# Performance work log

Measured on AMD Instinct MI355X. Metric: run time of the kernel, lower is better.

The kernel has to match this reference:

```python
import jax, jax.numpy as jnp
import numpy as np

N_NODES = 100000
N_EDGES = 1250000
N_FEAT = 64
HIDDEN = 16
N_CLASSES = 7


def setup_inputs() -> dict:
    key = jax.random.key(0)
    ks = jax.random.split(key, 10)
    x = jax.random.normal(ks[0], (N_NODES, N_FEAT), dtype=jnp.float32)
    edge_index = jax.random.randint(ks[1], (2, N_EDGES), 0, N_NODES, dtype=jnp.int64)
    s = 0.1
    return {
        "x": x,
        "edge_index": edge_index,
        # conv1 MLP: Linear(F,16) ReLU Linear(16,16) ReLU
        "W1": jax.random.normal(ks[2], (N_FEAT, HIDDEN), dtype=jnp.float32) * s,
        "b1": jnp.zeros((HIDDEN,), dtype=jnp.float32),
        "W2": jax.random.normal(ks[3], (HIDDEN, HIDDEN), dtype=jnp.float32) * s,
        "b2": jnp.zeros((HIDDEN,), dtype=jnp.float32),
        # conv2 MLP: Linear(16,16) ReLU Linear(16,C)
        "W3": jax.random.normal(ks[4], (HIDDEN, HIDDEN), dtype=jnp.float32) * s,
        "b3": jnp.zeros((HIDDEN,), dtype=jnp.float32),
        "W4": jax.random.normal(ks[5], (HIDDEN, N_CLASSES), dtype=jnp.float32) * s,
        "b4": jnp.zeros((N_CLASSES,), dtype=jnp.float32),
    }


def _gin_aggregate(h, src, dst):
    # GINConv with default eps=0: (1+eps)*x + sum_{j in N(i)} x_j
    msgs = h[src]  # [E, d] gather
    agg = jax.ops.segment_sum(msgs, dst, num_segments=h.shape[0])  # scatter-add
    return h + agg


def reference(x, edge_index, W1, b1, W2, b2, W3, b3, W4, b4):
    src = edge_index[0]
    dst = edge_index[1]
    # conv1: GIN aggregate + MLP(Linear,ReLU,Linear,ReLU)
    h = _gin_aggregate(x, src, dst)
    h = jax.nn.relu(h @ W1 + b1)
    h = jax.nn.relu(h @ W2 + b2)
    # F.relu after conv1 (idempotent here, kept for faithfulness)
    h = jax.nn.relu(h)
    # conv2: GIN aggregate + MLP(Linear,ReLU,Linear)
    h = _gin_aggregate(h, src, dst)
    h = jax.nn.relu(h @ W3 + b3)
    h = h @ W4 + b4
    return jax.nn.log_softmax(h, axis=1)
```

## Files before the change

### kernel.cpp

```cpp
#include <hip/hip_runtime.h>
#include <math.h>

constexpr int NN = 100000;
constexpr int NE = 1250000;
constexpr int NF = 64;
constexpr int NH = 16;
constexpr int NC = 7;

constexpr int BKT_SHIFT = 7;
constexpr int BKT_NODES = 1 << BKT_SHIFT;
constexpr int NBUCKET = (NN + BKT_NODES - 1) / BKT_NODES;
constexpr int BSTRIDE = 2048;
constexpr int EPB = 8192;
constexpr int NBLK_BUCKET = (NE + EPB - 1) / EPB;
constexpr int NBLK_PAD = 160;

__global__ __launch_bounds__(256) void k1_gemm(
    const float* __restrict__ x, const float* __restrict__ W1,
    float* __restrict__ A) {
    __shared__ float w[NF * NH];
    for (int i = threadIdx.x; i < NF * NH; i += blockDim.x) w[i] = W1[i];
    __syncthreads();
    int node = blockIdx.x * 256 + threadIdx.x;
    if (node >= NN) return;

    float acc[NH];
#pragma unroll
    for (int j = 0; j < NH; ++j) acc[j] = 0.f;

    const float4* xr = (const float4*)(x + (size_t)node * NF);
#pragma unroll
    for (int k4 = 0; k4 < NF / 4; ++k4) {
        float4 xv = xr[k4];
        int k = k4 * 4;
#pragma unroll
        for (int j = 0; j < NH; ++j) {
            acc[j] += xv.x * w[(k + 0) * NH + j]
                    + xv.y * w[(k + 1) * NH + j]
                    + xv.z * w[(k + 2) * NH + j]
                    + xv.w * w[(k + 3) * NH + j];
        }
    }
    float4* Ar = (float4*)(A + (size_t)node * NH);
#pragma unroll
    for (int q = 0; q < NH / 4; ++q) {
        float4 a;
        a.x = acc[q * 4 + 0]; a.y = acc[q * 4 + 1];
        a.z = acc[q * 4 + 2]; a.w = acc[q * 4 + 3];
        Ar[q] = a;
    }
}

__global__ __launch_bounds__(1024) void k_count(
    const int* __restrict__ dst, int* __restrict__ gcnt) {
    __shared__ int cnt[NBUCKET];
    int tid = threadIdx.x;
    for (int i = tid; i < NBUCKET; i += 1024) cnt[i] = 0;
    __syncthreads();
    int base = blockIdx.x * EPB;
#pragma unroll
    for (int k = 0; k < 8; ++k) {
        int e = base + k * 1024 + tid;
        if (e < NE) atomicAdd(&cnt[dst[e] >> BKT_SHIFT], 1);
    }
    __syncthreads();
    for (int i = tid; i < NBUCKET; i += 1024)
        gcnt[i * NBLK_PAD + blockIdx.x] = cnt[i];
}

__global__ __launch_bounds__(256) void k_base(
    const int* __restrict__ gcnt, int* __restrict__ gbase, int* __restrict__ tcnt) {
    __shared__ int s[256];
    int b = blockIdx.x;
    int tid = threadIdx.x;
    int v = (tid < NBLK_BUCKET) ? gcnt[b * NBLK_PAD + tid] : 0;
    s[tid] = v;
    __syncthreads();
    for (int d = 1; d < 256; d <<= 1) {
        int u = (tid >= d) ? s[tid - d] : 0;
        __syncthreads();
        s[tid] += u;
        __syncthreads();
    }
    if (tid < NBLK_BUCKET) gbase[b * NBLK_PAD + tid] = s[tid] - v;
    if (tid == 255) tcnt[b] = s[255];
}

__global__ __launch_bounds__(1024) void k_scatter(
    const int* __restrict__ src, const int* __restrict__ dst,
    const int* __restrict__ gbase, unsigned* __restrict__ gbuf) {
    __shared__ int cnt[NBUCKET];
    __shared__ int loff[NBUCKET];
    __shared__ int gb[NBUCKET];
    __shared__ int s[1024];
    __shared__ unsigned sorted[EPB];
    __shared__ unsigned short sortedB[EPB];

    int tid = threadIdx.x;
    for (int i = tid; i < NBUCKET; i += 1024) {
        cnt[i] = 0;
        gb[i] = gbase[i * NBLK_PAD + blockIdx.x];
    }
    __syncthreads();

    unsigned pk[8];
    int bk[8];
    int rk[8];
    int base = blockIdx.x * EPB;
    int nval = NE - base; if (nval > EPB) nval = EPB;
#pragma unroll
    for (int k = 0; k < 8; ++k) {
        int e = base + k * 1024 + tid;
        bk[k] = -1;
        if (e < NE) {
            int sv = src[e];
            int d = dst[e];
            int b = d >> BKT_SHIFT;
            bk[k] = b;
            pk[k] = ((unsigned)sv << BKT_SHIFT) | (unsigned)(d & (BKT_NODES - 1));
            rk[k] = atomicAdd(&cnt[b], 1);
        }
    }
    __syncthreads();

    int v = (tid < NBUCKET) ? cnt[tid] : 0;
    s[tid] = v;
    __syncthreads();
    for (int d = 1; d < 1024; d <<= 1) {
        int u = (tid >= d) ? s[tid - d] : 0;
        __syncthreads();
        s[tid] += u;
        __syncthreads();
    }
    if (tid < NBUCKET) loff[tid] = s[tid] - v;
    __syncthreads();

#pragma unroll
    for (int k = 0; k < 8; ++k) {
        if (bk[k] >= 0) {
            int p = loff[bk[k]] + rk[k];
            sorted[p] = pk[k];
            sortedB[p] = (unsigned short)bk[k];
        }
    }
    __syncthreads();

    for (int i = tid; i < nval; i += 1024) {
        int b = sortedB[i];
        int pos = gb[b] + (i - loff[b]);
        if (pos < BSTRIDE)
            gbuf[(size_t)b * BSTRIDE + pos] = sorted[i];
    }
}

__global__ __launch_bounds__(512) void k_agg1(
    const float* __restrict__ A, float* __restrict__ A2,
    const int* __restrict__ tcnt, unsigned* __restrict__ gbuf,
    unsigned short* __restrict__ soff, unsigned short* __restrict__ scnt,
    const float* __restrict__ b1,
    const float* __restrict__ W2, const float* __restrict__ b2,
    const float* __restrict__ W3) {
    __shared__ unsigned stage[BSTRIDE];
    __shared__ unsigned eSrc[BSTRIDE];
    __shared__ int cnt[BKT_NODES], off[BKT_NODES], cur[BKT_NODES];
    __shared__ float Bl[BKT_NODES * 17];
    __shared__ float Tl[BKT_NODES * 17];
    __shared__ float w2[NH * NH], w3[NH * NH], bb1[NH], bb2[NH];

    int b = blockIdx.x;
    int tid = threadIdx.x;
    for (int i = tid; i < NH * NH; i += 512) { w2[i] = W2[i]; w3[i] = W3[i]; }
    if (tid < NH) { bb1[tid] = b1[tid]; bb2[tid] = b2[tid]; }
    int n = tcnt[b];
    if (n > BSTRIDE) n = BSTRIDE;
    if (tid < BKT_NODES) cnt[tid] = 0;
    __syncthreads();

    for (int i = tid; i < n; i += 512) {
        unsigned u = gbuf[(size_t)b * BSTRIDE + i];
        stage[i] = u;
        atomicAdd(&cnt[u & (BKT_NODES - 1)], 1);
    }
    __syncthreads();
    if (tid < BKT_NODES) off[tid] = cnt[tid];
    __syncthreads();
    for (int d = 1; d < BKT_NODES; d <<= 1) {
        int v = 0;
        if (tid < BKT_NODES && tid >= d) v = off[tid - d];
        __syncthreads();
        if (tid < BKT_NODES) off[tid] += v;
        __syncthreads();
    }
    if (tid < BKT_NODES) {
        int st = off[tid] - cnt[tid];
        cur[tid] = st;
        soff[b * BKT_NODES + tid] = (unsigned short)st;
        scnt[b * BKT_NODES + tid] = (unsigned short)cnt[tid];
    }
    __syncthreads();
    for (int i = tid; i < n; i += 512) {
        unsigned u = stage[i];
        int pos = atomicAdd(&cur[u & (BKT_NODES - 1)], 1);
        eSrc[pos] = u >> BKT_SHIFT;
    }
    __syncthreads();

    for (int i = tid; i < n; i += 512) gbuf[(size_t)b * BSTRIDE + i] = eSrc[i];

    int node = tid >> 2;
    int q = (tid & 3) * 4;
    int gnode = (b << BKT_SHIFT) + node;
    int end = off[node];
    int start = end - cnt[node];

    float4 bq = {0.f, 0.f, 0.f, 0.f};
    if (gnode < NN) bq = *(const float4*)(A + (size_t)gnode * NH + q);
    float4 a0 = {0.f, 0.f, 0.f, 0.f}, a1 = {0.f, 0.f, 0.f, 0.f};
    int j = start;
    for (; j + 2 <= end; j += 2) {
        int s0 = eSrc[j];
        int s1 = eSrc[j + 1];
        float4 v0 = *(const float4*)(A + (size_t)s0 * NH + q);
        float4 v1 = *(const float4*)(A + (size_t)s1 * NH + q);
        a0.x += v0.x; a0.y += v0.y; a0.z += v0.z; a0.w += v0.w;
        a1.x += v1.x; a1.y += v1.y; a1.z += v1.z; a1.w += v1.w;
    }
    if (j < end) {
        int s0 = eSrc[j];
        float4 v0 = *(const float4*)(A + (size_t)s0 * NH + q);
        a0.x += v0.x; a0.y += v0.y; a0.z += v0.z; a0.w += v0.w;
    }
    Bl[node * 17 + q + 0] = fmaxf(bq.x + bb1[q + 0] + a0.x + a1.x, 0.f);
    Bl[node * 17 + q + 1] = fmaxf(bq.y + bb1[q + 1] + a0.y + a1.y, 0.f);
    Bl[node * 17 + q + 2] = fmaxf(bq.z + bb1[q + 2] + a0.z + a1.z, 0.f);
    Bl[node * 17 + q + 3] = fmaxf(bq.w + bb1[q + 3] + a0.w + a1.w, 0.f);
    __syncthreads();

    float t0 = bb2[q], t1 = bb2[q + 1], t2 = bb2[q + 2], t3 = bb2[q + 3];
#pragma unroll
    for (int k = 0; k < NH; ++k) {
        float hk = Bl[node * 17 + k];
        t0 += hk * w2[k * NH + q + 0];
        t1 += hk * w2[k * NH + q + 1];
        t2 += hk * w2[k * NH + q + 2];
        t3 += hk * w2[k * NH + q + 3];
    }
    Tl[node * 17 + q + 0] = fmaxf(t0, 0.f);
    Tl[node * 17 + q + 1] = fmaxf(t1, 0.f);
    Tl[node * 17 + q + 2] = fmaxf(t2, 0.f);
    Tl[node * 17 + q + 3] = fmaxf(t3, 0.f);
    __syncthreads();

    float z0 = 0.f, z1 = 0.f, z2 = 0.f, z3 = 0.f;
#pragma unroll
    for (int k = 0; k < NH; ++k) {
        float tk = Tl[node * 17 + k];
        z0 += tk * w3[k * NH + q + 0];
        z1 += tk * w3[k * NH + q + 1];
        z2 += tk * w3[k * NH + q + 2];
        z3 += tk * w3[k * NH + q + 3];
    }
    if (gnode < NN) {
        float4 az = {z0, z1, z2, z3};
        *(float4*)(A2 + (size_t)gnode * NH + q) = az;
    }
}

__global__ __launch_bounds__(512) void k_agg2(
    const float* __restrict__ A2,
    const int* __restrict__ tcnt, const unsigned* __restrict__ gbuf,
    const unsigned short* __restrict__ soff, const unsigned short* __restrict__ scnt,
    const float* __restrict__ b3,
    const float* __restrict__ W4, const float* __restrict__ b4,
    float* __restrict__ out) {
    __shared__ unsigned eSrc[BSTRIDE];
    __shared__ int off[BKT_NODES], cnt[BKT_NODES];
    __shared__ float Bl[BKT_NODES * 17];
    __shared__ float w4[NH * NC];
    __shared__ float bb3[NH];
    __shared__ float bb4[NC];

    int b = blockIdx.x;
    int tid = threadIdx.x;
    for (int i = tid; i < NH * NC; i += 512) w4[i] = W4[i];
    if (tid < NH) bb3[tid] = b3[tid];
    if (tid < NC) bb4[tid] = b4[tid];
    int n = tcnt[b];
    if (n > BSTRIDE) n = BSTRIDE;
    if (tid < BKT_NODES) {
        off[tid] = soff[b * BKT_NODES + tid];
        cnt[tid] = scnt[b * BKT_NODES + tid];
    }
    for (int i = tid; i < n; i += 512) eSrc[i] = gbuf[(size_t)b * BSTRIDE + i];
    __syncthreads();

    int node = tid >> 2;
    int q = (tid & 3) * 4;
    int gnode = (b << BKT_SHIFT) + node;
    int start = off[node];
    int end = start + cnt[node];

    float4 bq = {0.f, 0.f, 0.f, 0.f};
    if (gnode < NN) bq = *(const float4*)(A2 + (size_t)gnode * NH + q);
    float4 a0 = {0.f, 0.f, 0.f, 0.f}, a1 = {0.f, 0.f, 0.f, 0.f};
    int j = start;
    for (; j + 2 <= end; j += 2) {
        int s0 = eSrc[j];
        int s1 = eSrc[j + 1];
        float4 v0 = *(const float4*)(A2 + (size_t)s0 * NH + q);
        float4 v1 = *(const float4*)(A2 + (size_t)s1 * NH + q);
        a0.x += v0.x; a0.y += v0.y; a0.z += v0.z; a0.w += v0.w;
        a1.x += v1.x; a1.y += v1.y; a1.z += v1.z; a1.w += v1.w;
    }
    if (j < end) {
        int s0 = eSrc[j];
        float4 v0 = *(const float4*)(A2 + (size_t)s0 * NH + q);
        a0.x += v0.x; a0.y += v0.y; a0.z += v0.z; a0.w += v0.w;
    }
    Bl[node * 17 + q + 0] = fmaxf(bq.x + bb3[q + 0] + a0.x + a1.x, 0.f);
    Bl[node * 17 + q + 1] = fmaxf(bq.y + bb3[q + 1] + a0.y + a1.y, 0.f);
    Bl[node * 17 + q + 2] = fmaxf(bq.z + bb3[q + 2] + a0.z + a1.z, 0.f);
    Bl[node * 17 + q + 3] = fmaxf(bq.w + bb3[q + 3] + a0.w + a1.w, 0.f);
    __syncthreads();

    if (tid < BKT_NODES) {
        int nd = tid;
        int gn = (b << BKT_SHIFT) + nd;
        if (gn < NN) {
            float o[NC];
#pragma unroll
            for (int c = 0; c < NC; ++c) o[c] = bb4[c];
#pragma unroll
            for (int k = 0; k < NH; ++k) {
                float hk = Bl[nd * 17 + k];
#pragma unroll
                for (int c = 0; c < NC; ++c) o[c] += hk * w4[k * NC + c];
            }
            float m = o[0];
#pragma unroll
            for (int c = 1; c < NC; ++c) m = fmaxf(m, o[c]);
            float s = 0.f;
#pragma unroll
            for (int c = 0; c < NC; ++c) s += expf(o[c] - m);
            float ls = m + logf(s);
            float* op = out + (size_t)gn * NC;
#pragma unroll
            for (int c = 0; c < NC; ++c) op[c] = o[c] - ls;
        }
    }
}

extern "C" void kernel_launch(void* const* d_in, const int* in_sizes, int n_in,
                              void* d_out, int out_size, void* d_ws, size_t ws_size,
                              hipStream_t stream) {
    const float* x  = (const float*)d_in[0];
    const int*   ei = (const int*)d_in[1];
    const float* W1 = (const float*)d_in[2];
    const float* b1 = (const float*)d_in[3];
    const float* W2 = (const float*)d_in[4];
    const float* b2 = (const float*)d_in[5];
    const float* W3 = (const float*)d_in[6];
    const float* b3 = (const float*)d_in[7];
    const float* W4 = (const float*)d_in[8];
    const float* b4 = (const float*)d_in[9];
    float* out = (float*)d_out;

    const int* src = ei;
    const int* dst = ei + NE;

    float*          A    = (float*)d_ws;
    float*          A2   = A + (size_t)NN * NH;
    unsigned*       gbuf = (unsigned*)(A2 + (size_t)NN * NH);
    int*            gcnt = (int*)(gbuf + (size_t)NBUCKET * BSTRIDE);
    int*            gbase= gcnt + (size_t)NBUCKET * NBLK_PAD;
    int*            tcnt = gbase + (size_t)NBUCKET * NBLK_PAD;
    unsigned short* soff = (unsigned short*)(tcnt + ((NBUCKET + 3) & ~3));
    unsigned short* scnt = soff + (size_t)NBUCKET * BKT_NODES;

    const int nodeBlocks = (NN + 255) / 256;

    k1_gemm<<<nodeBlocks, 256, 0, stream>>>(x, W1, A);
    k_count<<<NBLK_BUCKET, 1024, 0, stream>>>(dst, gcnt);
    k_base<<<NBUCKET, 256, 0, stream>>>(gcnt, gbase, tcnt);
    k_scatter<<<NBLK_BUCKET, 1024, 0, stream>>>(src, dst, gbase, gbuf);
    k_agg1<<<NBUCKET, 512, 0, stream>>>(A, A2, tcnt, gbuf, soff, scnt, b1, W2, b2, W3);
    k_agg2<<<NBUCKET, 512, 0, stream>>>(A2, tcnt, gbuf, soff, scnt, b3, W4, b4, out);
}
```

Measured before the change: 74.76 us.

## Fuse edge counting into first GEMM, halve scatter chunk, use wave-shuffle scans

```diff
diff --git a/kernel.cpp b/kernel.cpp
--- a/kernel.cpp
+++ b/kernel.cpp
@@ -11,15 +11,44 @@
 constexpr int BKT_NODES = 1 << BKT_SHIFT;
 constexpr int NBUCKET = (NN + BKT_NODES - 1) / BKT_NODES;
 constexpr int BSTRIDE = 2048;
-constexpr int EPB = 8192;
+constexpr int EPB = 4096;
 constexpr int NBLK_BUCKET = (NE + EPB - 1) / EPB;
-constexpr int NBLK_PAD = 160;
-
-__global__ __launch_bounds__(256) void k1_gemm(
+constexpr int NBLK_PAD = 320;
+constexpr int EPC = 4096;
+constexpr int NBLK_COUNT = (NE + EPC - 1) / EPC;
+constexpr int NODE_BLOCKS = (NN + 255) / 256;
+
+__device__ __forceinline__ int wave_iscan(int v, int lane) {
+#pragma unroll
+    for (int d = 1; d < 64; d <<= 1) {
+        int u = __shfl_up(v, d, 64);
+        if (lane >= d) v += u;
+    }
+    return v;
+}
+
+__global__ __launch_bounds__(256) void k1_fused(
     const float* __restrict__ x, const float* __restrict__ W1,
-    float* __restrict__ A) {
+    float* __restrict__ A, const int* __restrict__ dst, int* __restrict__ gcnt) {
+    if (blockIdx.x >= NODE_BLOCKS) {
+        __shared__ int cnt[NBUCKET];
+        int blk = blockIdx.x - NODE_BLOCKS;
+        int tid = threadIdx.x;
+        for (int i = tid; i < NBUCKET; i += 256) cnt[i] = 0;
+        __syncthreads();
+        int base = blk * EPC;
+#pragma unroll
+        for (int k = 0; k < EPC / 256; ++k) {
+            int e = base + k * 256 + tid;
+            if (e < NE) atomicAdd(&cnt[dst[e] >> BKT_SHIFT], 1);
+        }
+        __syncthreads();
+        for (int i = tid; i < NBUCKET; i += 256)
+            gcnt[i * NBLK_PAD + blk] = cnt[i];
+        return;
+    }
     __shared__ float w[NF * NH];
-    for (int i = threadIdx.x; i < NF * NH; i += blockDim.x) w[i] = W1[i];
+    for (int i = threadIdx.x; i < NF * NH; i += 256) w[i] = W1[i];
     __syncthreads();
     int node = blockIdx.x * 256 + threadIdx.x;
     if (node >= NN) return;
@@ -51,39 +80,25 @@
     }
 }
 
-__global__ __launch_bounds__(1024) void k_count(
-    const int* __restrict__ dst, int* __restrict__ gcnt) {
-    __shared__ int cnt[NBUCKET];
-    int tid = threadIdx.x;
-    for (int i = tid; i < NBUCKET; i += 1024) cnt[i] = 0;
-    __syncthreads();
-    int base = blockIdx.x * EPB;
-#pragma unroll
-    for (int k = 0; k < 8; ++k) {
-        int e = base + k * 1024 + tid;
-        if (e < NE) atomicAdd(&cnt[dst[e] >> BKT_SHIFT], 1);
-    }
-    __syncthreads();
-    for (int i = tid; i < NBUCKET; i += 1024)
-        gcnt[i * NBLK_PAD + blockIdx.x] = cnt[i];
-}
-
-__global__ __launch_bounds__(256) void k_base(
+__global__ __launch_bounds__(320) void k_base(
     const int* __restrict__ gcnt, int* __restrict__ gbase, int* __restrict__ tcnt) {
-    __shared__ int s[256];
+    __shared__ int wsum[5];
     int b = blockIdx.x;
     int tid = threadIdx.x;
-    int v = (tid < NBLK_BUCKET) ? gcnt[b * NBLK_PAD + tid] : 0;
-    s[tid] = v;
-    __syncthreads();
-    for (int d = 1; d < 256; d <<= 1) {
-        int u = (tid >= d) ? s[tid - d] : 0;
-        __syncthreads();
-        s[tid] += u;
-        __syncthreads();
-    }
-    if (tid < NBLK_BUCKET) gbase[b * NBLK_PAD + tid] = s[tid] - v;
-    if (tid == 255) tcnt[b] = s[255];
+    int lane = tid & 63, wid = tid >> 6;
+    int v = (tid < NBLK_COUNT) ? gcnt[b * NBLK_PAD + tid] : 0;
+    int sv = wave_iscan(v, lane);
+    if (lane == 63) wsum[wid] = sv;
+    __syncthreads();
+    if (wid == 0) {
+        int wv = (lane < 5) ? wsum[lane] : 0;
+        int ws = wave_iscan(wv, lane);
+        if (lane < 5) wsum[lane] = ws - wv;
+    }
+    __syncthreads();
+    int excl = sv - v + wsum[wid];
+    if (tid < NBLK_COUNT) gbase[b * NBLK_PAD + tid] = excl;
+    if (tid == NBLK_COUNT - 1) tcnt[b] = excl + v;
 }
 
 __global__ __launch_bounds__(1024) void k_scatter(
@@ -92,7 +107,7 @@
     __shared__ int cnt[NBUCKET];
     __shared__ int loff[NBUCKET];
     __shared__ int gb[NBUCKET];
-    __shared__ int s[1024];
+    __shared__ int wsum[16];
     __shared__ unsigned sorted[EPB];
     __shared__ unsigned short sortedB[EPB];
 
@@ -103,13 +118,13 @@
     }
     __syncthreads();
 
-    unsigned pk[8];
-    int bk[8];
-    int rk[8];
+    unsigned pk[EPB / 1024];
+    int bk[EPB / 1024];
+    int rk[EPB / 1024];
     int base = blockIdx.x * EPB;
     int nval = NE - base; if (nval > EPB) nval = EPB;
 #pragma unroll
-    for (int k = 0; k < 8; ++k) {
+    for (int k = 0; k < EPB / 1024; ++k) {
         int e = base + k * 1024 + tid;
         bk[k] = -1;
         if (e < NE) {
@@ -123,20 +138,22 @@
     }
     __syncthreads();
 
+    int lane = tid & 63, wid = tid >> 6;
     int v = (tid < NBUCKET) ? cnt[tid] : 0;
-    s[tid] = v;
-    __syncthreads();
-    for (int d = 1; d < 1024; d <<= 1) {
-        int u = (tid >= d) ? s[tid - d] : 0;
-        __syncthreads();
-        s[tid] += u;
-        __syncthreads();
-    }
-    if (tid < NBUCKET) loff[tid] = s[tid] - v;
-    __syncthreads();
-
-#pragma unroll
-    for (int k = 0; k < 8; ++k) {
+    int sv = wave_iscan(v, lane);
+    if (lane == 63) wsum[wid] = sv;
+    __syncthreads();
+    if (wid == 0) {
+        int wv = (lane < 16) ? wsum[lane] : 0;
+        int ws = wave_iscan(wv, lane);
+        if (lane < 16) wsum[lane] = ws - wv;
+    }
+    __syncthreads();
+    if (tid < NBUCKET) loff[tid] = sv - v + wsum[wid];
+    __syncthreads();
+
+#pragma unroll
+    for (int k = 0; k < EPB / 1024; ++k) {
         if (bk[k] >= 0) {
             int p = loff[bk[k]] + rk[k];
             sorted[p] = pk[k];
@@ -163,6 +180,7 @@
     __shared__ unsigned stage[BSTRIDE];
     __shared__ unsigned eSrc[BSTRIDE];
     __shared__ int cnt[BKT_NODES], off[BKT_NODES], cur[BKT_NODES];
+    __shared__ int wtot[2];
     __shared__ float Bl[BKT_NODES * 17];
     __shared__ float Tl[BKT_NODES * 17];
     __shared__ float w2[NH * NH], w3[NH * NH], bb1[NH], bb2[NH];
@@ -182,20 +200,23 @@
         atomicAdd(&cnt[u & (BKT_NODES - 1)], 1);
     }
     __syncthreads();
-    if (tid < BKT_NODES) off[tid] = cnt[tid];
-    __syncthreads();
-    for (int d = 1; d < BKT_NODES; d <<= 1) {
-        int v = 0;
-        if (tid < BKT_NODES && tid >= d) v = off[tid - d];
-        __syncthreads();
-        if (tid < BKT_NODES) off[tid] += v;
-        __syncthreads();
-    }
+
+    int lane = tid & 63, wid = tid >> 6;
+    int sv = 0, v = 0;
     if (tid < BKT_NODES) {
-        int st = off[tid] - cnt[tid];
+        v = cnt[tid];
+        sv = wave_iscan(v, lane);
+        if (lane == 63) wtot[wid] = sv;
+    }
+    __syncthreads();
+    if (tid < BKT_NODES) {
+        int add = (wid == 1) ? wtot[0] : 0;
+        int inc = sv + add;
+        off[tid] = inc;
+        int st = inc - v;
         cur[tid] = st;
         soff[b * BKT_NODES + tid] = (unsigned short)st;
-        scnt[b * BKT_NODES + tid] = (unsigned short)cnt[tid];
+        scnt[b * BKT_NODES + tid] = (unsigned short)v;
     }
     __syncthreads();
     for (int i = tid; i < n; i += 512) {
@@ -377,11 +398,8 @@
     unsigned short* soff = (unsigned short*)(tcnt + ((NBUCKET + 3) & ~3));
     unsigned short* scnt = soff + (size_t)NBUCKET * BKT_NODES;
 
-    const int nodeBlocks = (NN + 255) / 256;
-
-    k1_gemm<<<nodeBlocks, 256, 0, stream>>>(x, W1, A);
-    k_count<<<NBLK_BUCKET, 1024, 0, stream>>>(dst, gcnt);
-    k_base<<<NBUCKET, 256, 0, stream>>>(gcnt, gbase, tcnt);
+    k1_fused<<<NODE_BLOCKS + NBLK_COUNT, 256, 0, stream>>>(x, W1, A, dst, gcnt);
+    k_base<<<NBUCKET, 320, 0, stream>>>(gcnt, gbase, tcnt);
     k_scatter<<<NBLK_BUCKET, 1024, 0, stream>>>(src, dst, gbase, gbuf);
     k_agg1<<<NBUCKET, 512, 0, stream>>>(A, A2, tcnt, gbuf, soff, scnt, b1, W2, b2, W3);
     k_agg2<<<NBUCKET, 512, 0, stream>>>(A2, tcnt, gbuf, soff, scnt, b3, W4, b4, out);
```

Result: no change. 74.95 us (+0.2%).
